# Optimization experiments

Measured on AMD Instinct MI355X. Metric: run time of the kernel, lower is better.

The kernel has to match this reference:

```python
import jax, jax.numpy as jnp
import numpy as np

B, S, D, H = 2, 2048, 1024, 16
DK = D // H


def layernorm(x, gamma, bias, eps=1e-6):
    m = jnp.mean(x, axis=-1, keepdims=True)
    v = jnp.mean((x - m) ** 2, axis=-1, keepdims=True)  # biased var (correction=0)
    return gamma * (x - m) / jnp.sqrt(v + eps) + bias


def setup_inputs() -> dict:
    key = jax.random.key(0)
    ks = jax.random.split(key, 10)
    xav = (2.0 / (D + D)) ** 0.5  # xavier_normal_ std for square [D,D]
    lin1_b = (1.0 / D) ** 0.5     # nn.Linear default init bound
    lin2_b = (1.0 / (4 * D)) ** 0.5
    return {
        "X": jax.random.normal(ks[0], (B, S, D), jnp.float32),
        "padding_mask": jnp.ones((B, 1, S), jnp.int32),
        "W_Q": jax.random.normal(ks[1], (D, D), jnp.float32) * xav,
        "W_K": jax.random.normal(ks[2], (D, D), jnp.float32) * xav,
        "W_V": jax.random.normal(ks[3], (D, D), jnp.float32) * xav,
        "W_O": jax.random.normal(ks[4], (D, D), jnp.float32) * xav,
        "g1": jnp.ones((D,), jnp.float32),
        "b1": jnp.zeros((D,), jnp.float32),
        "W1": jax.random.uniform(ks[5], (D, 4 * D), jnp.float32, -lin1_b, lin1_b),
        "bias1": jax.random.uniform(ks[6], (4 * D,), jnp.float32, -lin1_b, lin1_b),
        "W2": jax.random.uniform(ks[7], (4 * D, D), jnp.float32, -lin2_b, lin2_b),
        "bias2": jax.random.uniform(ks[8], (D,), jnp.float32, -lin2_b, lin2_b),
        "g2": jnp.ones((D,), jnp.float32),
        "b2": jnp.zeros((D,), jnp.float32),
    }


def reference(X, padding_mask, W_Q, W_K, W_V, W_O, g1, b1, W1, bias1, W2, bias2, g2, b2):
    b, s, d = X.shape
    # pre-norm + MHA
    xn = layernorm(X, g1, b1)
    q = (xn @ W_Q).reshape(b, s, H, DK).transpose(0, 2, 1, 3)  # [B,H,S,DK]
    k = (xn @ W_K).reshape(b, s, H, DK).transpose(0, 2, 1, 3)
    v = (xn @ W_V).reshape(b, s, H, DK).transpose(0, 2, 1, 3)
    scores = jnp.einsum("bhqd,bhkd->bhqk", q, k) / np.sqrt(DK).astype(np.float32)
    mask = padding_mask[:, None, :, :]  # [B,1,1,S] broadcast over heads/queries
    scores = jnp.where(mask == 0, jnp.float32(-1e9), scores)
    w = jax.nn.softmax(scores, axis=-1)
    attn = jnp.einsum("bhqk,bhkd->bhqd", w, v)
    attn = attn.transpose(0, 2, 1, 3).reshape(b, s, d) @ W_O
    out = attn + X
    # pre-norm + GELU FFN (exact erf GELU, matching nn.GELU default)
    nn2 = layernorm(out, g2, b2)
    ff = jax.nn.gelu(nn2 @ W1 + bias1, approximate=False) @ W2 + bias2
    return ff + out
```

## Files before the change

kernel.cpp:

```cpp
#include <hip/hip_runtime.h>
#include <hip/hip_bf16.h>


using bf16 = __hip_bfloat16;
typedef __attribute__((ext_vector_type(4))) float f32x4;
typedef __attribute__((ext_vector_type(16))) float f32x16;
typedef __attribute__((ext_vector_type(8))) short bf16x8;

#define DEVI static __device__ __forceinline__

DEVI void async_copy16(const void* g, void* l) {
  __builtin_amdgcn_global_load_lds(
      (const __attribute__((address_space(1))) void*)g,
      (__attribute__((address_space(3))) void*)l, 16, 0, 0);
}

DEVI ushort f2bf_bits(float v) {
  __hip_bfloat16 h = __float2bfloat16(v);
  return *reinterpret_cast<ushort*>(&h);
}

DEVI float bfbits2f(ushort u) {
  union { float f; unsigned int i; } x;
  x.i = ((unsigned int)u) << 16;
  return x.f;
}

DEVI unsigned int pk2(float lo, float hi) {
  return (unsigned int)f2bf_bits(lo) | ((unsigned int)f2bf_bits(hi) << 16);
}

__global__ __launch_bounds__(256) void transpose_all_ln(
    const float* __restrict__ q, const float* __restrict__ k,
    const float* __restrict__ v, const float* __restrict__ o,
    const float* __restrict__ w1, const float* __restrict__ w2,
    bf16* __restrict__ wqkvo, bf16* __restrict__ w1t, bf16* __restrict__ w2t,
    const float* __restrict__ X, const float* __restrict__ g1,
    const float* __restrict__ b1, bf16* __restrict__ xn) {
  const int tid = blockIdx.x;
  if (tid >= 12288) {
    const long row = tid - 12288;
    const int t = threadIdx.x;
    float4 x = ((const float4*)(X + row * 1024))[t];
    float s = x.x + x.y + x.z + x.w;
    float s2 = x.x * x.x + x.y * x.y + x.z * x.z + x.w * x.w;
#pragma unroll
    for (int m = 1; m < 64; m <<= 1) {
      s += __shfl_xor(s, m);
      s2 += __shfl_xor(s2, m);
    }
    __shared__ float red[8];
    const int w = t >> 6, l = t & 63;
    if (l == 0) { red[w] = s; red[4 + w] = s2; }
    __syncthreads();
    s = red[0] + red[1] + red[2] + red[3];
    s2 = red[4] + red[5] + red[6] + red[7];
    const float mean = s * (1.0f / 1024.0f);
    const float var = s2 * (1.0f / 1024.0f) - mean * mean;
    const float rstd = rsqrtf(var + 1e-6f);
    float4 g4 = ((const float4*)g1)[t];
    float4 b4 = ((const float4*)b1)[t];
    union { ushort h[4]; uint2 u; } oo;
    oo.h[0] = f2bf_bits(g4.x * (x.x - mean) * rstd + b4.x);
    oo.h[1] = f2bf_bits(g4.y * (x.y - mean) * rstd + b4.y);
    oo.h[2] = f2bf_bits(g4.z * (x.z - mean) * rstd + b4.z);
    oo.h[3] = f2bf_bits(g4.w * (x.w - mean) * rstd + b4.w);
    ((uint2*)(xn + row * 1024))[t] = oo.u;
    return;
  }
  const float* W;
  bf16* Wt;
  int K, N, n0, k0;
  if (tid < 4096) {
    const int z = tid >> 10, r = tid & 1023;
    W = (z == 0) ? q : (z == 1) ? k : (z == 2) ? v : o;
    Wt = wqkvo + (size_t)z * 1024 * 1024;
    K = 1024; N = 1024; n0 = (r & 31) << 5; k0 = (r >> 5) << 5;
  } else if (tid < 8192) {
    const int r = tid - 4096;
    W = w1; Wt = w1t; K = 1024; N = 4096;
    n0 = (r & 127) << 5; k0 = (r >> 7) << 5;
  } else {
    const int r = tid - 8192;
    W = w2; Wt = w2t; K = 4096; N = 1024;
    n0 = (r & 31) << 5; k0 = (r >> 5) << 5;
  }
  __shared__ float tile[32][33];
  const int tx = threadIdx.x & 31, ty = threadIdx.x >> 5;
#pragma unroll
  for (int i = 0; i < 32; i += 8)
    tile[ty + i][tx] = W[(long)(k0 + ty + i) * N + n0 + tx];
  __syncthreads();
#pragma unroll
  for (int i = 0; i < 32; i += 8)
    Wt[(long)(n0 + ty + i) * K + k0 + tx] = __float2bfloat16(tile[tx][ty + i]);
}

__global__ __launch_bounds__(256) void oproj_reduce_ln(
    const float* __restrict__ p0, const float* __restrict__ p1,
    const float* __restrict__ X, const float* __restrict__ gamma,
    const float* __restrict__ beta, float* __restrict__ res_out,
    bf16* __restrict__ xn_out) {
  const long row = blockIdx.x;
  const int t = threadIdx.x;
  const long i = row * 256 + t;
  const float4 a = ((const float4*)p0)[i];
  const float4 b = ((const float4*)p1)[i];
  const float4 c = ((const float4*)X)[i];
  float4 x;
  x.x = a.x + b.x + c.x; x.y = a.y + b.y + c.y;
  x.z = a.z + b.z + c.z; x.w = a.w + b.w + c.w;
  ((float4*)res_out)[i] = x;
  float s = x.x + x.y + x.z + x.w;
  float s2 = x.x * x.x + x.y * x.y + x.z * x.z + x.w * x.w;
#pragma unroll
  for (int m = 1; m < 64; m <<= 1) {
    s += __shfl_xor(s, m);
    s2 += __shfl_xor(s2, m);
  }
  __shared__ float red[8];
  const int w = t >> 6, l = t & 63;
  if (l == 0) { red[w] = s; red[4 + w] = s2; }
  __syncthreads();
  s = red[0] + red[1] + red[2] + red[3];
  s2 = red[4] + red[5] + red[6] + red[7];
  const float mean = s * (1.0f / 1024.0f);
  const float var = s2 * (1.0f / 1024.0f) - mean * mean;
  const float rstd = rsqrtf(var + 1e-6f);
  float4 g4 = ((const float4*)gamma)[t];
  float4 b4 = ((const float4*)beta)[t];
  union { ushort h[4]; uint2 u; } o;
  o.h[0] = f2bf_bits(g4.x * (x.x - mean) * rstd + b4.x);
  o.h[1] = f2bf_bits(g4.y * (x.y - mean) * rstd + b4.y);
  o.h[2] = f2bf_bits(g4.z * (x.z - mean) * rstd + b4.z);
  o.h[3] = f2bf_bits(g4.w * (x.w - mean) * rstd + b4.w);
  ((uint2*)(xn_out + row * 1024))[t] = o.u;
}

template <int EPI, int KSPLIT>
__global__ __launch_bounds__(256) void gemm_bt(
    const bf16* __restrict__ A, const bf16* __restrict__ Bt,
    const int M, const int N, const int K, const int lda, const int ldb,
    const float* __restrict__ bias, const float* __restrict__ res,
    float* __restrict__ pother, void* __restrict__ Cout) {
  __shared__ __align__(16) char gsmem[81920];
  const int t = threadIdx.x;
  const int w = t >> 6, l = t & 63;
  const int nb = N >> 7;
  const int cpx = gridDim.x >> 3;
  int bidx = (blockIdx.x & 7) * cpx + (blockIdx.x >> 3);
  int sl = 0;
  if (KSPLIT == 2) {
    const int half = gridDim.x >> 1;
    sl = bidx >= half;
    bidx -= sl * half;
  }
  const int bm = bidx / nb, bn = bidx % nb;
  const long row0 = (long)bm << 7, col0 = (long)bn << 7;
  const int wr = (w >> 1) << 6, wc = (w & 1) << 6;
  const int lr = l & 15;
  const int lkb = (l >> 4) << 4;

  f32x4 acc[4][4];
#pragma unroll
  for (int m = 0; m < 4; ++m)
#pragma unroll
    for (int n = 0; n < 4; ++n) acc[m][n] = (f32x4){0.f, 0.f, 0.f, 0.f};

  const int rA = t >> 3;
  const int g = (t & 7) ^ ((t >> 3) & 7);
  const bf16* gA = A + (row0 + rA) * (long)lda + (long)sl * K + g * 8;
  const bf16* gB = Bt + (col0 + rA) * (long)ldb + (long)sl * K + g * 8;
  char* const Bbase = gsmem + 49152;

  const int nt = K >> 6;
#pragma unroll
  for (int cr = 0; cr < 4; ++cr)
    async_copy16(gA + (long)cr * 32 * lda, gsmem + t * 16 + cr * 4096);
#pragma unroll
  for (int cr = 0; cr < 4; ++cr)
    async_copy16(gB + (long)cr * 32 * ldb, Bbase + t * 16 + cr * 4096);
#pragma unroll
  for (int cr = 0; cr < 4; ++cr)
    async_copy16(gA + (long)cr * 32 * lda + 64, gsmem + 16384 + t * 16 + cr * 4096);
  int curB = 0;

  for (int kt = 0; kt < nt; ++kt) {
    if (kt + 1 < nt) {
      const int k1 = (kt + 1) << 6;
      char* dstB = Bbase + (curB ^ 1) * 16384;
#pragma unroll
      for (int cr = 0; cr < 4; ++cr)
        async_copy16(gB + (long)cr * 32 * ldb + k1, dstB + t * 16 + cr * 4096);
    }
    if (kt + 2 < nt) {
      const int k2 = (kt + 2) << 6;
      char* dstA = gsmem + ((kt + 2) % 3) * 16384;
#pragma unroll
      for (int cr = 0; cr < 4; ++cr)
        async_copy16(gA + (long)cr * 32 * lda + k2, dstA + t * 16 + cr * 4096);
    }
    if (kt < nt - 2) {
      asm volatile("s_waitcnt vmcnt(12)" ::: "memory");
    } else if (kt == nt - 2) {
      asm volatile("s_waitcnt vmcnt(8)" ::: "memory");
    } else {
      asm volatile("s_waitcnt vmcnt(0)" ::: "memory");
    }
    __builtin_amdgcn_s_barrier();
    __builtin_amdgcn_sched_barrier(0);
    const char* As = gsmem + (kt % 3) * 16384;
    const char* Bs = Bbase + curB * 16384;
#pragma unroll
    for (int ks = 0; ks < 2; ++ks) {
      bf16x8 af[4], bfr[4];
#pragma unroll
      for (int m = 0; m < 4; ++m) {
        const int row = wr + m * 16 + lr;
        af[m] = *(const bf16x8*)(As +
            (row * 128 + ((ks * 64 + lkb) ^ ((row & 7) << 4))));
      }
#pragma unroll
      for (int n = 0; n < 4; ++n) {
        const int row = wc + n * 16 + lr;
        bfr[n] = *(const bf16x8*)(Bs +
            (row * 128 + ((ks * 64 + lkb) ^ ((row & 7) << 4))));
      }
#pragma unroll
      for (int m = 0; m < 4; ++m)
#pragma unroll
        for (int n = 0; n < 4; ++n)
          acc[m][n] = __builtin_amdgcn_mfma_f32_16x16x32_bf16(af[m], bfr[n], acc[m][n], 0, 0, 0);
    }
    __builtin_amdgcn_sched_barrier(0);
    __builtin_amdgcn_s_barrier();
    curB ^= 1;
  }

  bf16* Cb = (bf16*)Cout;
  float* Cf = (float*)Cout;
  if ((EPI == 4 || EPI == 5) && sl == 1) Cf = pother;
#pragma unroll
  for (int m = 0; m < 4; ++m) {
#pragma unroll
    for (int r = 0; r < 4; ++r) {
      const long crow = row0 + wr + m * 16 + ((l >> 4) << 2) + r;
      const long rbase = crow * N;
#pragma unroll
      for (int n = 0; n < 4; ++n) {
        const long ccol = col0 + wc + n * 16 + lr;
        float v = acc[m][n][r];
        if (EPI == 2) {
          const float vv = v + bias[ccol];
          const float u2 = vv * (1.5957691216f + 0.0713548162f * vv * vv);
          v = vv / (1.0f + __expf(-u2));
        }
        if (EPI == 5 && sl == 0) v += bias[ccol] + res[rbase + ccol];
        if (EPI == 0 || EPI == 2)
          Cb[rbase + ccol] = __float2bfloat16(v);
        else
          Cf[rbase + ccol] = v;
      }
    }
  }
}

__global__ __launch_bounds__(256) void ff2_reduce(
    const float* __restrict__ p0, const float* __restrict__ p1,
    float* __restrict__ out) {
  const int idx = blockIdx.x * 256 + threadIdx.x;
  const float4 x = ((const float4*)p0)[idx];
  const float4 y = ((const float4*)p1)[idx];
  float4 a;
  a.x = x.x + y.x; a.y = x.y + y.y; a.z = x.z + y.z; a.w = x.w + y.w;
  ((float4*)out)[idx] = a;
}

__global__ __launch_bounds__(512) void attn_kernel(
    const bf16* __restrict__ QKV, const int* __restrict__ pmask,
    bf16* __restrict__ Oout) {
  const int bh = blockIdx.x;
  const int b = bh >> 4, h = bh & 15;
  const int q0 = blockIdx.y << 8;
  const int t = threadIdx.x;
  const int w = t >> 6, l = t & 63;
  const int lq = l & 31, hi = l >> 5;

  __shared__ __align__(16) char smem[65536];

  const long base = (long)b * 2048 * 3072;
  const bf16* Qg = QKV + base + h * 64;
  const bf16* Kg = QKV + base + 1024 + h * 64;
  const bf16* Vg = QKV + base + 2048 + h * 64;

  int kSrc[2], kDst[2], vk[2], vsg[2];
#pragma unroll
  for (int p = 0; p < 2; ++p) {
    const int c = p * 512 + t;
    const int kr = c >> 3;
    kSrc[p] = kr * 3072 + (((c & 7) ^ (kr & 7)) << 3);
    kDst[p] = c * 16;
    vk[p] = c >> 3;
    vsg[p] = c & 7;
  }

  const int qw0 = q0 + w * 32;
  bf16x8 qf[4];
#pragma unroll
  for (int dc = 0; dc < 4; ++dc) {
    uint4 raw = *(const uint4*)(Qg + (long)(qw0 + lq) * 3072 + dc * 16 + hi * 8);
    union { uint4 u4; ushort us[8]; } in; in.u4 = raw;
    union { bf16x8 v; ushort us[8]; } o;
#pragma unroll
    for (int e = 0; e < 8; ++e) o.us[e] = f2bf_bits(0.125f * bfbits2f(in.us[e]));
    qf[dc] = o.v;
  }

  union { unsigned int u[4]; bf16x8 v; } bones;
  bones.u[0] = (hi == 0) ? 0x00003F80u : 0u;
  bones.u[1] = bones.u[2] = bones.u[3] = 0u;

  uint4 vreg[2];
#pragma unroll
  for (int p = 0; p < 2; ++p) {
    vreg[p] = *(const uint4*)(Vg + (long)vk[p] * 3072 + vsg[p] * 8);
    async_copy16(Kg + kSrc[p], smem + kDst[p]);
  }
#pragma unroll
  for (int p = 0; p < 2; ++p) {
    const ushort* vs = (const ushort*)&vreg[p];
#pragma unroll
    for (int e = 0; e < 8; ++e) {
      const int d = vsg[p] * 8 + e;
      *(ushort*)(smem + 32768 + d * 256 +
                 ((vk[p] * 2) ^ (((e ^ vsg[p]) & 7) << 4))) = vs[e];
    }
  }

  f32x16 oacc[2];
#pragma unroll
  for (int nt = 0; nt < 2; ++nt)
#pragma unroll
    for (int r = 0; r < 16; ++r) oacc[nt][r] = 0.f;
  float mrun = -3.0e38f, lsum = 0.f;
  int cur = 0;

  __syncthreads();

  for (int ktg = 0; ktg < 16; ++ktg) {
    if (ktg < 15) {
      const long nrow0 = (long)(ktg + 1) * 128 * 3072;
#pragma unroll
      for (int p = 0; p < 2; ++p) {
        vreg[p] = *(const uint4*)(Vg + nrow0 + (long)vk[p] * 3072 + vsg[p] * 8);
        async_copy16(Kg + nrow0 + kSrc[p], smem + (cur ^ 1) * 16384 + kDst[p]);
      }
    }
    const int k0 = ktg << 7;
    const char* Ks = smem + cur * 16384;
    const char* Vt = smem + 32768 + cur * 16384;

    f32x16 sacc[4];
    __builtin_amdgcn_s_setprio(1);
#pragma unroll
    for (int kt = 0; kt < 4; ++kt) {
#pragma unroll
      for (int r = 0; r < 16; ++r) sacc[kt][r] = 0.f;
#pragma unroll
      for (int dc = 0; dc < 4; ++dc) {
        bf16x8 ka = *(const bf16x8*)(Ks +
            ((kt * 32 + lq) * 128 + ((dc * 32 + hi * 16) ^ ((lq & 7) << 4))));
        sacc[kt] = __builtin_amdgcn_mfma_f32_32x32x16_bf16(ka, qf[dc], sacc[kt], 0, 0, 0);
      }
      const int mv = pmask[b * 2048 + k0 + kt * 32 + lq];
      union { unsigned int u[4]; bf16x8 v; } aadd;
      aadd.u[0] = (hi == 0 && mv == 0) ? (unsigned int)f2bf_bits(-1.0e9f) : 0u;
      aadd.u[1] = aadd.u[2] = aadd.u[3] = 0u;
      sacc[kt] = __builtin_amdgcn_mfma_f32_32x32x16_bf16(aadd.v, bones.v, sacc[kt], 0, 0, 0);
    }
    __builtin_amdgcn_s_setprio(0);

    float tmax = -3.0e38f;
#pragma unroll
    for (int kt = 0; kt < 4; ++kt)
#pragma unroll
      for (int r = 0; r < 16; ++r) tmax = fmaxf(tmax, sacc[kt][r]);
    tmax = fmaxf(tmax, __shfl_xor(tmax, 32));
    const bool need = (bool)__any(tmax > mrun + 8.0f);
    const float mnew = need ? fmaxf(mrun, tmax) : mrun;
    float psum = 0.f;
#pragma unroll
    for (int kt = 0; kt < 4; ++kt)
#pragma unroll
      for (int r = 0; r < 16; ++r) {
        const float p = __expf(sacc[kt][r] - mnew);
        sacc[kt][r] = p;
        psum += p;
      }
    psum += __shfl_xor(psum, 32);
    if (need) {
      const float alpha = __expf(mrun - mnew);
      mrun = mnew;
      lsum = lsum * alpha + psum;
#pragma unroll
      for (int r = 0; r < 16; ++r) {
        const float ar = __shfl(alpha, (r & 3) + 8 * (r >> 2) + 4 * hi);
        oacc[0][r] *= ar;
        oacc[1][r] *= ar;
      }
    } else {
      lsum += psum;
    }

    union { unsigned int u[4]; bf16x8 v; } paE[4], paO[4];
#pragma unroll
    for (int kt = 0; kt < 4; ++kt) {
      unsigned int c0 = pk2(sacc[kt][0], sacc[kt][1]);
      unsigned int c1 = pk2(sacc[kt][2], sacc[kt][3]);
      unsigned int c2 = pk2(sacc[kt][4], sacc[kt][5]);
      unsigned int c3 = pk2(sacc[kt][6], sacc[kt][7]);
      unsigned int c4 = pk2(sacc[kt][8], sacc[kt][9]);
      unsigned int c5 = pk2(sacc[kt][10], sacc[kt][11]);
      unsigned int c6 = pk2(sacc[kt][12], sacc[kt][13]);
      unsigned int c7 = pk2(sacc[kt][14], sacc[kt][15]);
      asm volatile("v_permlane32_swap_b32 %0, %1" : "+v"(c0), "+v"(c2));
      asm volatile("v_permlane32_swap_b32 %0, %1" : "+v"(c1), "+v"(c3));
      asm volatile("v_permlane32_swap_b32 %0, %1" : "+v"(c4), "+v"(c6));
      asm volatile("v_permlane32_swap_b32 %0, %1" : "+v"(c5), "+v"(c7));
      paE[kt].u[0] = c0; paE[kt].u[1] = c1; paE[kt].u[2] = c2; paE[kt].u[3] = c3;
      paO[kt].u[0] = c4; paO[kt].u[1] = c5; paO[kt].u[2] = c6; paO[kt].u[3] = c7;
    }

    __builtin_amdgcn_s_setprio(1);
#pragma unroll
    for (int kt = 0; kt < 4; ++kt)
#pragma unroll
      for (int nt = 0; nt < 2; ++nt) {
        const int vrow = nt * 32 + lq;
        const int vsw = ((vrow & 7) ^ ((vrow >> 3) & 7)) << 4;
        bf16x8 vbE = *(const bf16x8*)(Vt + (vrow * 256 + ((kt * 64 + hi * 16) ^ vsw)));
        oacc[nt] = __builtin_amdgcn_mfma_f32_32x32x16_bf16(paE[kt].v, vbE, oacc[nt], 0, 0, 0);
        bf16x8 vbO = *(const bf16x8*)(Vt + (vrow * 256 + ((kt * 64 + 32 + hi * 16) ^ vsw)));
        oacc[nt] = __builtin_amdgcn_mfma_f32_32x32x16_bf16(paO[kt].v, vbO, oacc[nt], 0, 0, 0);
      }
    __builtin_amdgcn_s_setprio(0);

    if (ktg < 15) {
      char* VtN = smem + 32768 + (cur ^ 1) * 16384;
#pragma unroll
      for (int p = 0; p < 2; ++p) {
        const ushort* vs = (const ushort*)&vreg[p];
#pragma unroll
        for (int e = 0; e < 8; ++e) {
          const int d = vsg[p] * 8 + e;
          *(ushort*)(VtN + d * 256 +
                     ((vk[p] * 2) ^ (((e ^ vsg[p]) & 7) << 4))) = vs[e];
        }
      }
    }

    __syncthreads();
    cur ^= 1;
  }

  const float inv = 1.0f / lsum;
#pragma unroll
  for (int r = 0; r < 16; ++r) {
    const int crow = (r & 3) + 8 * (r >> 2) + 4 * hi;
    const float ir = __shfl(inv, crow);
    const long orow = (long)b * 2048 + qw0 + crow;
#pragma unroll
    for (int nt = 0; nt < 2; ++nt)
      Oout[orow * 1024 + h * 64 + nt * 32 + lq] = __float2bfloat16(oacc[nt][r] * ir);
  }
}

extern "C" void kernel_launch(void* const* d_in, const int* in_sizes, int n_in,
                              void* d_out, int out_size, void* d_ws, size_t ws_size,
                              hipStream_t stream) {
  const float* X = (const float*)d_in[0];
  const int* pmask = (const int*)d_in[1];
  const float* W_Q = (const float*)d_in[2];
  const float* W_K = (const float*)d_in[3];
  const float* W_V = (const float*)d_in[4];
  const float* W_O = (const float*)d_in[5];
  const float* g1 = (const float*)d_in[6];
  const float* b1 = (const float*)d_in[7];
  const float* W1 = (const float*)d_in[8];
  const float* bias1 = (const float*)d_in[9];
  const float* W2 = (const float*)d_in[10];
  const float* bias2 = (const float*)d_in[11];
  const float* g2 = (const float*)d_in[12];
  const float* b2 = (const float*)d_in[13];
  (void)in_sizes; (void)n_in; (void)out_size; (void)ws_size;

  char* ws = (char*)d_ws;
  const size_t MB = 1ull << 20;
  bf16* W1_t   = (bf16*)(ws + 0);
  bf16* Wqkv_t = (bf16*)(ws + 8 * MB);
  bf16* Wo_t   = (bf16*)(ws + 14 * MB);
  bf16* W2_t   = (bf16*)(ws + 16 * MB);
  bf16* xn     = (bf16*)(ws + 24 * MB);
  bf16* QKV    = (bf16*)(ws + 32 * MB);
  bf16* attnb  = (bf16*)(ws + 56 * MB);
  bf16* ff1    = (bf16*)(ws + 32 * MB);
  float* p0o   = (float*)(ws + 64 * MB);
  float* p1o   = (float*)(ws + 32 * MB);
  float* p0    = (float*)(ws + 64 * MB);
  float* p1    = (float*)(ws + 0);
  float* res1  = (float*)d_out;

  transpose_all_ln<<<16384, 256, 0, stream>>>(W_Q, W_K, W_V, W_O, W1, W2,
                                              Wqkv_t, W1_t, W2_t,
                                              X, g1, b1, xn);
  gemm_bt<0, 1><<<32 * 24, 256, 0, stream>>>(xn, Wqkv_t, 4096, 3072, 1024, 1024, 1024,
                                             nullptr, nullptr, nullptr, QKV);
  attn_kernel<<<dim3(32, 8), 512, 0, stream>>>(QKV, pmask, attnb);
  gemm_bt<4, 2><<<2 * 32 * 8, 256, 0, stream>>>(attnb, Wo_t, 4096, 1024, 512, 1024, 1024,
                                                nullptr, nullptr, p1o, p0o);
  oproj_reduce_ln<<<4096, 256, 0, stream>>>(p0o, p1o, X, g2, b2, res1, xn);
  gemm_bt<2, 1><<<32 * 32, 256, 0, stream>>>(xn, W1_t, 4096, 4096, 1024, 1024, 1024,
                                             bias1, nullptr, nullptr, ff1);
  gemm_bt<5, 2><<<2 * 32 * 8, 256, 0, stream>>>(ff1, W2_t, 4096, 1024, 2048, 4096, 4096,
                                                bias2, res1, p1, p0);
  ff2_reduce<<<4096, 256, 0, stream>>>(p0, p1, res1);
}
```

Before: 260.1 us.

## Software-pipeline QK^T of next tile with softmax, prefetch KV two tiles ahead

Restructures the attention loop so the QK^T MFMAs for tile t+1 are issued before the softmax and PV work of tile t. This lets matrix math overlap the exp/max/sum VALU work. V is now triple-buffered in LDS, and K and V loads are prefetched two tiles ahead, which raises LDS use from 64KB to 80KB. Launch bounds now request two blocks per CU. Holding two score accumulator sets under that occupancy bound raises register pressure and risks spills.

```diff
diff --git a/kernel.cpp b/kernel.cpp
--- a/kernel.cpp
+++ b/kernel.cpp
@@ -276,7 +276,7 @@
   ((float4*)out)[idx] = a;
 }
 
-__global__ __launch_bounds__(512) void attn_kernel(
+__global__ __launch_bounds__(512, 2) void attn_kernel(
     const bf16* __restrict__ QKV, const int* __restrict__ pmask,
     bf16* __restrict__ Oout) {
   const int bh = blockIdx.x;
@@ -286,7 +286,7 @@
   const int w = t >> 6, l = t & 63;
   const int lq = l & 31, hi = l >> 5;
 
-  __shared__ __align__(16) char smem[65536];
+  __shared__ __align__(16) char smem[81920];
 
   const long base = (long)b * 2048 * 3072;
   const bf16* Qg = QKV + base + h * 64;
@@ -336,6 +336,21 @@
                  ((vk[p] * 2) ^ (((e ^ vsg[p]) & 7) << 4))) = vs[e];
     }
   }
+#pragma unroll
+  for (int p = 0; p < 2; ++p) {
+    vreg[p] = *(const uint4*)(Vg + (long)(128 + vk[p]) * 3072 + vsg[p] * 8);
+    async_copy16(Kg + (long)128 * 3072 + kSrc[p], smem + 16384 + kDst[p]);
+  }
+#pragma unroll
+  for (int p = 0; p < 2; ++p) {
+    const ushort* vs = (const ushort*)&vreg[p];
+#pragma unroll
+    for (int e = 0; e < 8; ++e) {
+      const int d = vsg[p] * 8 + e;
+      *(ushort*)(smem + 32768 + 16384 + d * 256 +
+                 ((vk[p] * 2) ^ (((e ^ vsg[p]) & 7) << 4))) = vs[e];
+    }
+  }
 
   f32x16 oacc[2];
 #pragma unroll
@@ -343,48 +358,46 @@
 #pragma unroll
     for (int r = 0; r < 16; ++r) oacc[nt][r] = 0.f;
   float mrun = -3.0e38f, lsum = 0.f;
-  int cur = 0;
-
-  __syncthreads();
-
-  for (int ktg = 0; ktg < 16; ++ktg) {
-    if (ktg < 15) {
-      const long nrow0 = (long)(ktg + 1) * 128 * 3072;
-#pragma unroll
-      for (int p = 0; p < 2; ++p) {
-        vreg[p] = *(const uint4*)(Vg + nrow0 + (long)vk[p] * 3072 + vsg[p] * 8);
-        async_copy16(Kg + nrow0 + kSrc[p], smem + (cur ^ 1) * 16384 + kDst[p]);
-      }
-    }
-    const int k0 = ktg << 7;
-    const char* Ks = smem + cur * 16384;
-    const char* Vt = smem + 32768 + cur * 16384;
-
-    f32x16 sacc[4];
+
+  auto qkt = [&](f32x16 (&s)[4], int tile) {
+    const char* Ks = smem + (tile & 1) * 16384;
     __builtin_amdgcn_s_setprio(1);
 #pragma unroll
     for (int kt = 0; kt < 4; ++kt) {
 #pragma unroll
-      for (int r = 0; r < 16; ++r) sacc[kt][r] = 0.f;
+      for (int r = 0; r < 16; ++r) s[kt][r] = 0.f;
 #pragma unroll
       for (int dc = 0; dc < 4; ++dc) {
         bf16x8 ka = *(const bf16x8*)(Ks +
             ((kt * 32 + lq) * 128 + ((dc * 32 + hi * 16) ^ ((lq & 7) << 4))));
-        sacc[kt] = __builtin_amdgcn_mfma_f32_32x32x16_bf16(ka, qf[dc], sacc[kt], 0, 0, 0);
-      }
-      const int mv = pmask[b * 2048 + k0 + kt * 32 + lq];
+        s[kt] = __builtin_amdgcn_mfma_f32_32x32x16_bf16(ka, qf[dc], s[kt], 0, 0, 0);
+      }
+      const int mv = pmask[b * 2048 + tile * 128 + kt * 32 + lq];
       union { unsigned int u[4]; bf16x8 v; } aadd;
       aadd.u[0] = (hi == 0 && mv == 0) ? (unsigned int)f2bf_bits(-1.0e9f) : 0u;
       aadd.u[1] = aadd.u[2] = aadd.u[3] = 0u;
-      sacc[kt] = __builtin_amdgcn_mfma_f32_32x32x16_bf16(aadd.v, bones.v, sacc[kt], 0, 0, 0);
+      s[kt] = __builtin_amdgcn_mfma_f32_32x32x16_bf16(aadd.v, bones.v, s[kt], 0, 0, 0);
     }
     __builtin_amdgcn_s_setprio(0);
+  };
+
+  auto iter = [&](f32x16 (&cur)[4], f32x16 (&nxt)[4], int tile) {
+    __syncthreads();
+    if (tile + 2 < 16) {
+      const long nrow0 = (long)(tile + 2) * 128 * 3072;
+#pragma unroll
+      for (int p = 0; p < 2; ++p) {
+        vreg[p] = *(const uint4*)(Vg + nrow0 + (long)vk[p] * 3072 + vsg[p] * 8);
+        async_copy16(Kg + nrow0 + kSrc[p], smem + (tile & 1) * 16384 + kDst[p]);
+      }
+    }
+    if (tile < 15) qkt(nxt, tile + 1);
 
     float tmax = -3.0e38f;
 #pragma unroll
     for (int kt = 0; kt < 4; ++kt)
 #pragma unroll
-      for (int r = 0; r < 16; ++r) tmax = fmaxf(tmax, sacc[kt][r]);
+      for (int r = 0; r < 16; ++r) tmax = fmaxf(tmax, cur[kt][r]);
     tmax = fmaxf(tmax, __shfl_xor(tmax, 32));
     const bool need = (bool)__any(tmax > mrun + 8.0f);
     const float mnew = need ? fmaxf(mrun, tmax) : mrun;
@@ -393,8 +406,8 @@
     for (int kt = 0; kt < 4; ++kt)
 #pragma unroll
       for (int r = 0; r < 16; ++r) {
-        const float p = __expf(sacc[kt][r] - mnew);
-        sacc[kt][r] = p;
+        const float p = __expf(cur[kt][r] - mnew);
+        cur[kt][r] = p;
         psum += p;
       }
     psum += __shfl_xor(psum, 32);
@@ -415,14 +428,14 @@
     union { unsigned int u[4]; bf16x8 v; } paE[4], paO[4];
 #pragma unroll
     for (int kt = 0; kt < 4; ++kt) {
-      unsigned int c0 = pk2(sacc[kt][0], sacc[kt][1]);
-      unsigned int c1 = pk2(sacc[kt][2], sacc[kt][3]);
-      unsigned int c2 = pk2(sacc[kt][4], sacc[kt][5]);
-      unsigned int c3 = pk2(sacc[kt][6], sacc[kt][7]);
-      unsigned int c4 = pk2(sacc[kt][8], sacc[kt][9]);
-      unsigned int c5 = pk2(sacc[kt][10], sacc[kt][11]);
-      unsigned int c6 = pk2(sacc[kt][12], sacc[kt][13]);
-      unsigned int c7 = pk2(sacc[kt][14], sacc[kt][15]);
+      unsigned int c0 = pk2(cur[kt][0], cur[kt][1]);
+      unsigned int c1 = pk2(cur[kt][2], cur[kt][3]);
+      unsigned int c2 = pk2(cur[kt][4], cur[kt][5]);
+      unsigned int c3 = pk2(cur[kt][6], cur[kt][7]);
+      unsigned int c4 = pk2(cur[kt][8], cur[kt][9]);
+      unsigned int c5 = pk2(cur[kt][10], cur[kt][11]);
+      unsigned int c6 = pk2(cur[kt][12], cur[kt][13]);
+      unsigned int c7 = pk2(cur[kt][14], cur[kt][15]);
       asm volatile("v_permlane32_swap_b32 %0, %1" : "+v"(c0), "+v"(c2));
       asm volatile("v_permlane32_swap_b32 %0, %1" : "+v"(c1), "+v"(c3));
       asm volatile("v_permlane32_swap_b32 %0, %1" : "+v"(c4), "+v"(c6));
@@ -431,6 +444,7 @@
       paO[kt].u[0] = c4; paO[kt].u[1] = c5; paO[kt].u[2] = c6; paO[kt].u[3] = c7;
     }
 
+    const char* Vt = smem + 32768 + (tile % 3) * 16384;
     __builtin_amdgcn_s_setprio(1);
 #pragma unroll
     for (int kt = 0; kt < 4; ++kt)
@@ -445,8 +459,8 @@
       }
     __builtin_amdgcn_s_setprio(0);
 
-    if (ktg < 15) {
-      char* VtN = smem + 32768 + (cur ^ 1) * 16384;
+    if (tile + 2 < 16) {
+      char* VtN = smem + 32768 + ((tile + 2) % 3) * 16384;
 #pragma unroll
       for (int p = 0; p < 2; ++p) {
         const ushort* vs = (const ushort*)&vreg[p];
@@ -458,9 +472,16 @@
         }
       }
     }
-
-    __syncthreads();
-    cur ^= 1;
+  };
+
+  __syncthreads();
+
+  f32x16 sacc0[4], sacc1[4];
+  qkt(sacc0, 0);
+
+  for (int tt = 0; tt < 8; ++tt) {
+    iter(sacc0, sacc1, 2 * tt);
+    iter(sacc1, sacc0, 2 * tt + 1);
   }
 
   const float inv = 1.0f / lsum;
```

Result: slower. 333.1 us (+28.1%).
